# Optimization experiments

Measured on AMD Instinct MI355X. Metric: run time of the kernel, lower is better.

Reference implementation:

```python
import jax, jax.numpy as jnp
import numpy as np
from jax import lax

# EmbedDims layout constants
OPCODE_START = 88
AX_START, PC_START, IMM_START = 163, 171, 195
BRANCH_TAKEN = 203
OP_JMP, OP_BZ, OP_BNZ = 2, 4, 5  # Opcode values


def setup_inputs() -> dict:
    key = jax.random.key(0)
    x = jax.random.normal(key, (16, 8192, 208), dtype=jnp.float32)
    return {"x": x}


def reference(x):
    # powers of 16 for nibble packing (16**7 = 2.68e8 fits fp32/int32 exactly)
    pw_f = jnp.float32(16.0) ** jnp.arange(8, dtype=jnp.float32)      # [8]
    pw_i = jnp.int32(16) ** jnp.arange(8, dtype=jnp.int32)            # [8]

    imm = jnp.einsum('...n,n->...', x[..., IMM_START:IMM_START + 8], pw_f)
    pc = jnp.einsum('...n,n->...', x[..., PC_START:PC_START + 8], pw_f)
    ax = (x[..., AX_START:AX_START + 8].astype(jnp.int32) * pw_i).sum(-1)
    ax_is_zero = ax == 0

    any_jmp = jnp.any(x[..., OPCODE_START + OP_JMP] > 0.5)
    any_bz = jnp.any(x[..., OPCODE_START + OP_BZ] > 0.5)
    any_bnz = jnp.any(x[..., OPCODE_START + OP_BNZ] > 0.5)

    def take_branch(x):
        # torch's global if/elif chain -> nested scalar-predicate wheres
        new_pc = jnp.where(
            any_jmp, imm,
            jnp.where(any_bz, jnp.where(ax_is_zero, imm, pc + 8.0),
                      jnp.where(any_bnz, jnp.where(~ax_is_zero, imm, pc + 8.0), pc)))
        bt = jnp.where(
            any_jmp, jnp.float32(1.0),
            jnp.where(any_bz, ax_is_zero.astype(x.dtype),
                      jnp.where(any_bnz, (~ax_is_zero).astype(x.dtype),
                                x[..., BRANCH_TAKEN])))
        shifts = jnp.arange(8, dtype=jnp.int32) * 4
        nibs = ((new_pc.astype(jnp.int32)[..., None] >> shifts) & 15).astype(x.dtype)  # [..., 8]
        out = x.at[..., BRANCH_TAKEN].set(bt)
        out = out.at[..., PC_START:PC_START + 8].set(nibs)
        return out

    # early-return branch: no JMP/BZ/BNZ anywhere -> x unchanged
    return lax.cond(any_jmp | any_bz | any_bnz, take_branch, lambda x: x, x)
```

## Files before the change

kernel.cpp:

```cpp
#include <hip/hip_runtime.h>

#define N_ROWS (16 * 8192)
#define NCH 208
#define CH_JMP 90
#define CH_BZ  92
#define CH_BNZ 93
#define AX_START 163
#define PC_START 171
#define IMM_START 195
#define BRANCH_TAKEN 203

typedef float vf4 __attribute__((ext_vector_type(4)));

#define FLAG_MAGIC 0x7F1A6501

__global__ __launch_bounds__(256) void cfe_flags_k(const float* __restrict__ x,
                                                   int* __restrict__ flags) {
    int r = blockIdx.x * blockDim.x + threadIdx.x;
    const float* rp = x + (size_t)r * NCH;
    bool j  = rp[CH_JMP] > 0.5f;
    bool z  = rp[CH_BZ]  > 0.5f;
    bool nz = rp[CH_BNZ] > 0.5f;
    int lane = threadIdx.x & 63;
    if (__any(j)  && lane == 0) flags[0] = FLAG_MAGIC;
    if (__any(z)  && lane == 0) flags[1] = FLAG_MAGIC;
    if (__any(nz) && lane == 0) flags[2] = FLAG_MAGIC;
}

__global__ __launch_bounds__(256) void cfe_main_k(const float* __restrict__ x,
                                                  float* __restrict__ out,
                                                  const int* __restrict__ flags) {
    int row  = (blockIdx.x << 2) | (threadIdx.x >> 6);
    int lane = threadIdx.x & 63;
    size_t base = (size_t)row * NCH;
    const vf4* src = (const vf4*)(x + base);

    vf4 v;
    if (lane < 52) v = src[lane];

    bool fj  = (flags[0] == FLAG_MAGIC);
    bool fz  = (flags[1] == FLAG_MAGIC);
    bool fnz = (flags[2] == FLAG_MAGIC);

    if (fj | fz | fnz) {
        const float* rp = x + base;
        float imm = 0.0f, pc = 0.0f;
        int   ax  = 0;
        float p   = 1.0f;
        int   pi  = 1;
#pragma unroll
        for (int i = 0; i < 8; ++i) {
            imm += rp[IMM_START + i] * p;
            pc  += rp[PC_START  + i] * p;
            ax  += ((int)rp[AX_START + i]) * pi;
            p  *= 16.0f;
            pi <<= 4;
        }
        bool az = (ax == 0);
        float new_pc, bt;
        if (fj)      { new_pc = imm;                        bt = 1.0f; }
        else if (fz) { new_pc = az ? imm : pc + 8.0f;       bt = az ? 1.0f : 0.0f; }
        else         { new_pc = az ? pc + 8.0f : imm;       bt = az ? 0.0f : 1.0f; }

        int ip = (int)new_pc;
        if (lane == 42) {
            v.w = (float)(ip & 15);
        } else if (lane == 43) {
            v.x = (float)((ip >>  4) & 15);
            v.y = (float)((ip >>  8) & 15);
            v.z = (float)((ip >> 12) & 15);
            v.w = (float)((ip >> 16) & 15);
        } else if (lane == 44) {
            v.x = (float)((ip >> 20) & 15);
            v.y = (float)((ip >> 24) & 15);
            v.z = (float)((ip >> 28) & 15);
        } else if (lane == 50) {
            v.w = bt;
        }
    }

    if (lane < 52) {
        __builtin_nontemporal_store(v, &((vf4*)(out + base))[lane]);
    }
}

extern "C" void kernel_launch(void* const* d_in, const int* in_sizes, int n_in,
                              void* d_out, int out_size, void* d_ws, size_t ws_size,
                              hipStream_t stream) {
    const float* x = (const float*)d_in[0];
    float* out     = (float*)d_out;
    int* flags     = (int*)d_ws;

    cfe_flags_k<<<N_ROWS / 256, 256, 0, stream>>>(x, flags);
    cfe_main_k<<<N_ROWS / 4, 256, 0, stream>>>(x, out, flags);
}
```

Measured before the change: 187.7 us.

## Fuse flag scan and row rewrite into one cooperative kernel with grid sync

Merges the flag-detection kernel and the main copy/rewrite kernel into a single cooperative launch of 512 blocks, separated by a grid-wide barrier. Each wave then streams 64 rows with a one-row register prefetch, and gathers the AX/PC/IMM nibbles through cross-lane shuffles instead of reloading them from global memory. This removes a second kernel launch and the redundant per-row scalar loads, at the cost of grid-sync overhead and lower parallelism: only 512 blocks of 256 threads, each wave working through its rows serially, which may underuse memory bandwidth.

```diff
diff --git a/kernel.cpp b/kernel.cpp
--- a/kernel.cpp
+++ b/kernel.cpp
@@ -1,86 +1,114 @@
 #include <hip/hip_runtime.h>
+#include <hip/hip_cooperative_groups.h>
+
+namespace cg = cooperative_groups;
 
 #define N_ROWS (16 * 8192)
 #define NCH 208
 #define CH_JMP 90
 #define CH_BZ  92
 #define CH_BNZ 93
-#define AX_START 163
-#define PC_START 171
-#define IMM_START 195
-#define BRANCH_TAKEN 203
 
 typedef float vf4 __attribute__((ext_vector_type(4)));
 
 #define FLAG_MAGIC 0x7F1A6501
 
-__global__ __launch_bounds__(256) void cfe_flags_k(const float* __restrict__ x,
+__global__ __launch_bounds__(256) void cfe_fused_k(const float* __restrict__ x,
+                                                   float* __restrict__ out,
                                                    int* __restrict__ flags) {
-    int r = blockIdx.x * blockDim.x + threadIdx.x;
-    const float* rp = x + (size_t)r * NCH;
-    bool j  = rp[CH_JMP] > 0.5f;
-    bool z  = rp[CH_BZ]  > 0.5f;
-    bool nz = rp[CH_BNZ] > 0.5f;
-    int lane = threadIdx.x & 63;
-    if (__any(j)  && lane == 0) flags[0] = FLAG_MAGIC;
-    if (__any(z)  && lane == 0) flags[1] = FLAG_MAGIC;
-    if (__any(nz) && lane == 0) flags[2] = FLAG_MAGIC;
-}
+    const int tid  = blockIdx.x * 256 + threadIdx.x;
+    const int lane = threadIdx.x & 63;
 
-__global__ __launch_bounds__(256) void cfe_main_k(const float* __restrict__ x,
-                                                  float* __restrict__ out,
-                                                  const int* __restrict__ flags) {
-    int row  = (blockIdx.x << 2) | (threadIdx.x >> 6);
-    int lane = threadIdx.x & 63;
-    size_t base = (size_t)row * NCH;
-    const vf4* src = (const vf4*)(x + base);
+    {
+        const float* rp = x + (size_t)tid * NCH;
+        bool j  = rp[CH_JMP] > 0.5f;
+        bool z  = rp[CH_BZ]  > 0.5f;
+        bool nz = rp[CH_BNZ] > 0.5f;
+        if (__any(j)  && lane == 0)
+            __hip_atomic_store(flags + 0, FLAG_MAGIC, __ATOMIC_RELAXED, __HIP_MEMORY_SCOPE_AGENT);
+        if (__any(z)  && lane == 0)
+            __hip_atomic_store(flags + 1, FLAG_MAGIC, __ATOMIC_RELAXED, __HIP_MEMORY_SCOPE_AGENT);
+        if (__any(nz) && lane == 0)
+            __hip_atomic_store(flags + 2, FLAG_MAGIC, __ATOMIC_RELAXED, __HIP_MEMORY_SCOPE_AGENT);
+    }
 
-    vf4 v;
+    cg::this_grid().sync();
+
+    const bool fj  = __hip_atomic_load(flags + 0, __ATOMIC_RELAXED, __HIP_MEMORY_SCOPE_AGENT) == FLAG_MAGIC;
+    const bool fz  = __hip_atomic_load(flags + 1, __ATOMIC_RELAXED, __HIP_MEMORY_SCOPE_AGENT) == FLAG_MAGIC;
+    const bool fnz = __hip_atomic_load(flags + 2, __ATOMIC_RELAXED, __HIP_MEMORY_SCOPE_AGENT) == FLAG_MAGIC;
+    const bool anyf = fj | fz | fnz;
+
+    const int gwave = tid >> 6;
+    const vf4* src = (const vf4*)(x   + (size_t)gwave * 64 * NCH);
+    vf4*       dst = (vf4*)      (out + (size_t)gwave * 64 * NCH);
+
+    vf4 v = {0.f, 0.f, 0.f, 0.f};
     if (lane < 52) v = src[lane];
 
-    bool fj  = (flags[0] == FLAG_MAGIC);
-    bool fz  = (flags[1] == FLAG_MAGIC);
-    bool fnz = (flags[2] == FLAG_MAGIC);
+#pragma unroll 4
+    for (int r = 0; r < 64; ++r) {
+        vf4 vn = {0.f, 0.f, 0.f, 0.f};
+        if (r < 63 && lane < 52) vn = src[(r + 1) * 52 + lane];
 
-    if (fj | fz | fnz) {
-        const float* rp = x + base;
-        float imm = 0.0f, pc = 0.0f;
-        int   ax  = 0;
-        float p   = 1.0f;
-        int   pi  = 1;
-#pragma unroll
-        for (int i = 0; i < 8; ++i) {
-            imm += rp[IMM_START + i] * p;
-            pc  += rp[PC_START  + i] * p;
-            ax  += ((int)rp[AX_START + i]) * pi;
-            p  *= 16.0f;
-            pi <<= 4;
+        if (anyf) {
+            float imm = 0.0f, pc = 0.0f;
+            int   ax  = 0;
+            float p   = 1.0f;
+            int   pi  = 1;
+
+            ax  += ((int)__shfl(v.w, 40)) * pi;
+            pc  += __shfl(v.w, 42) * p;
+            imm += __shfl(v.w, 48) * p;  pi <<= 4; p *= 16.0f;
+            ax  += ((int)__shfl(v.x, 41)) * pi;
+            pc  += __shfl(v.x, 43) * p;
+            imm += __shfl(v.x, 49) * p;  pi <<= 4; p *= 16.0f;
+            ax  += ((int)__shfl(v.y, 41)) * pi;
+            pc  += __shfl(v.y, 43) * p;
+            imm += __shfl(v.y, 49) * p;  pi <<= 4; p *= 16.0f;
+            ax  += ((int)__shfl(v.z, 41)) * pi;
+            pc  += __shfl(v.z, 43) * p;
+            imm += __shfl(v.z, 49) * p;  pi <<= 4; p *= 16.0f;
+            ax  += ((int)__shfl(v.w, 41)) * pi;
+            pc  += __shfl(v.w, 43) * p;
+            imm += __shfl(v.w, 49) * p;  pi <<= 4; p *= 16.0f;
+            ax  += ((int)__shfl(v.x, 42)) * pi;
+            pc  += __shfl(v.x, 44) * p;
+            imm += __shfl(v.x, 50) * p;  pi <<= 4; p *= 16.0f;
+            ax  += ((int)__shfl(v.y, 42)) * pi;
+            pc  += __shfl(v.y, 44) * p;
+            imm += __shfl(v.y, 50) * p;  pi <<= 4; p *= 16.0f;
+            ax  += ((int)__shfl(v.z, 42)) * pi;
+            pc  += __shfl(v.z, 44) * p;
+            imm += __shfl(v.z, 50) * p;
+
+            bool az = (ax == 0);
+            float new_pc, bt;
+            if (fj)      { new_pc = imm;                  bt = 1.0f; }
+            else if (fz) { new_pc = az ? imm : pc + 8.0f; bt = az ? 1.0f : 0.0f; }
+            else         { new_pc = az ? pc + 8.0f : imm; bt = az ? 0.0f : 1.0f; }
+
+            int ip = (int)new_pc;
+            if (lane == 42) {
+                v.w = (float)(ip & 15);
+            } else if (lane == 43) {
+                v.x = (float)((ip >>  4) & 15);
+                v.y = (float)((ip >>  8) & 15);
+                v.z = (float)((ip >> 12) & 15);
+                v.w = (float)((ip >> 16) & 15);
+            } else if (lane == 44) {
+                v.x = (float)((ip >> 20) & 15);
+                v.y = (float)((ip >> 24) & 15);
+                v.z = (float)((ip >> 28) & 15);
+            } else if (lane == 50) {
+                v.w = bt;
+            }
         }
-        bool az = (ax == 0);
-        float new_pc, bt;
-        if (fj)      { new_pc = imm;                        bt = 1.0f; }
-        else if (fz) { new_pc = az ? imm : pc + 8.0f;       bt = az ? 1.0f : 0.0f; }
-        else         { new_pc = az ? pc + 8.0f : imm;       bt = az ? 0.0f : 1.0f; }
 
-        int ip = (int)new_pc;
-        if (lane == 42) {
-            v.w = (float)(ip & 15);
-        } else if (lane == 43) {
-            v.x = (float)((ip >>  4) & 15);
-            v.y = (float)((ip >>  8) & 15);
-            v.z = (float)((ip >> 12) & 15);
-            v.w = (float)((ip >> 16) & 15);
-        } else if (lane == 44) {
-            v.x = (float)((ip >> 20) & 15);
-            v.y = (float)((ip >> 24) & 15);
-            v.z = (float)((ip >> 28) & 15);
-        } else if (lane == 50) {
-            v.w = bt;
+        if (lane < 52) {
+            __builtin_nontemporal_store(v, &dst[r * 52 + lane]);
         }
-    }
-
-    if (lane < 52) {
-        __builtin_nontemporal_store(v, &((vf4*)(out + base))[lane]);
+        v = vn;
     }
 }
 
@@ -91,6 +119,7 @@
     float* out     = (float*)d_out;
     int* flags     = (int*)d_ws;
 
-    cfe_flags_k<<<N_ROWS / 256, 256, 0, stream>>>(x, flags);
-    cfe_main_k<<<N_ROWS / 4, 256, 0, stream>>>(x, out, flags);
+    void* args[] = { (void*)&x, (void*)&out, (void*)&flags };
+    hipLaunchCooperativeKernel((const void*)cfe_fused_k,
+                               dim3(512), dim3(256), args, 0, stream);
 }
```

Result: slower. 440.3 us (+134.6%).
